# Kernel tuning notes

Measured on AMD Instinct MI355X. Metric: run time of the kernel, lower is better.

Reference implementation:

```python
import jax, jax.numpy as jnp
import numpy as np

PROJ = 8192     # projDim
THRESH = 1e-8   # numerical-stability epsilon for signed sqrt
L2_EPS = 1e-12  # eps of torch F.normalize


def setup_inputs() -> dict:
    key = jax.random.key(0)
    k1, k2, k3, k4, k5 = jax.random.split(key, 5)
    B, C, H, W = 16, 512, 14, 14
    x = jax.random.normal(k1, (B, C, H, W), dtype=jnp.float32)
    h1 = jax.random.randint(k2, (C,), 0, PROJ, dtype=jnp.int32)
    h2 = jax.random.randint(k3, (C,), 0, PROJ, dtype=jnp.int32)
    s1 = (2 * jax.random.randint(k4, (C,), 0, 2) - 1).astype(jnp.float32)
    s2 = (2 * jax.random.randint(k5, (C,), 0, 2) - 1).astype(jnp.float32)
    return {"x": x, "s1": s1, "s2": s2, "h1": h1, "h2": h2}


def reference(x, s1, s2, h1, h2):
    # x: [B, C, H, W]; h*: [C] hash buckets in [0, PROJ); s*: [C] signs (+-1)
    B, C, H, W = x.shape
    x_flat = jnp.transpose(x, (0, 2, 3, 1)).reshape(-1, C)  # [N, C], N = B*H*W

    def count_sketch(s, h):
        # Equivalent to x_flat @ M with M[c, h[c]] = s[c]: scatter-add of
        # sign-weighted channels into PROJ bins.  -> [N, PROJ]
        return jax.ops.segment_sum((x_flat * s).T, h, num_segments=PROJ).T

    fft1 = jnp.fft.fft(count_sketch(s1, h1), axis=-1)
    fft2 = jnp.fft.fft(count_sketch(s2, h2), axis=-1)
    conv = jnp.fft.ifft(fft1 * fft2, axis=-1).real       # [N, PROJ]
    y = conv.reshape(B, H, W, PROJ).sum(axis=(1, 2))      # sum pool -> [B, PROJ]
    y = jnp.sign(y) * jnp.sqrt(jnp.abs(y) + THRESH)       # signed sqrt
    norm = jnp.linalg.norm(y, axis=1, keepdims=True)
    return y / jnp.maximum(norm, L2_EPS)                  # l2 normalize (dim=1)
```

## Files before the change

kernel.cpp:

```cpp
#include <hip/hip_runtime.h>
#include <math.h>

#define PROJ 8192
#define NB   16
#define NC   512
#define HW   196

#define TB   128
#define KCH  20
#define LSA  24
#define LSB  36

__global__ void cbp_zero_ssq(float* __restrict__ ssq) {
    if (threadIdx.x < NB) ssq[threadIdx.x] = 0.0f;
}

__global__ __launch_bounds__(256)
void cbp_gram_scatter(const float* __restrict__ x,
                      const float* __restrict__ s1,
                      const float* __restrict__ s2,
                      const int*   __restrict__ h1,
                      const int*   __restrict__ h2,
                      float* __restrict__ ws) {
    __shared__ float sk[PROJ];
    __shared__ float As[TB * LSA];
    __shared__ float Bs[TB * LSB];

    const int blk = blockIdx.x;
    const int b = blk >> 4;
    const int I = (blk >> 2) & 3;
    const int J = blk & 3;
    const int c1base = I * TB;
    const int c2base = J * TB;

    const int tid = threadIdx.x;
    const int tx = tid & 15;
    const int ty = tid >> 4;

    for (int i = tid; i < PROJ; i += 256) sk[i] = 0.0f;

    const float* xa = x + ((size_t)b * NC + c1base) * HW;
    const float* xb = x + ((size_t)b * NC + c2base) * HW;

    float acc[8][8] = {{0.f}};

    for (int k0 = 0; k0 < HW; k0 += KCH) {
        const int kc = (k0 + KCH <= HW) ? KCH : (HW - k0);
        const int kq = kc >> 2;

        __syncthreads();
        for (int e = tid; e < TB * (KCH / 4); e += 256) {
            const int r = e / (KCH / 4);
            const int q = e - r * (KCH / 4);
            if (q < kq) {
                const float4 a4 = *(const float4*)&xa[r * HW + k0 + 4 * q];
                const float4 b4 = *(const float4*)&xb[r * HW + k0 + 4 * q];
                *(float4*)&As[r * LSA + 4 * q] = a4;
                *(float4*)&Bs[r * LSB + 4 * q] = b4;
            }
        }
        __syncthreads();

        for (int k = 0; k < kc; k += 4) {
            float4 av[8], bv[8];
#pragma unroll
            for (int i = 0; i < 8; i++)
                av[i] = *(const float4*)&As[(ty + 16 * i) * LSA + k];
#pragma unroll
            for (int j = 0; j < 8; j++)
                bv[j] = *(const float4*)&Bs[(tx + 16 * j) * LSB + k];
#pragma unroll
            for (int i = 0; i < 8; i++)
#pragma unroll
                for (int j = 0; j < 8; j++) {
                    acc[i][j] += av[i].x * bv[j].x;
                    acc[i][j] += av[i].y * bv[j].y;
                    acc[i][j] += av[i].z * bv[j].z;
                    acc[i][j] += av[i].w * bv[j].w;
                }
        }
    }
    __syncthreads();

    int   ha[8], hb[8];
    float sa[8], sb[8];
#pragma unroll
    for (int i = 0; i < 8; i++) {
        const int c1 = c1base + ty + 16 * i;
        ha[i] = h1[c1];  sa[i] = s1[c1];
    }
#pragma unroll
    for (int j = 0; j < 8; j++) {
        const int c2 = c2base + tx + 16 * j;
        hb[j] = h2[c2];  sb[j] = s2[c2];
    }
#pragma unroll
    for (int i = 0; i < 8; i++)
#pragma unroll
        for (int j = 0; j < 8; j++) {
            const int bin = (ha[i] + hb[j]) & (PROJ - 1);
            atomicAdd(&sk[bin], sa[i] * sb[j] * acc[i][j]);
        }
    __syncthreads();

    float4* dst = (float4*)(ws + (size_t)blk * PROJ);
    const float4* src = (const float4*)sk;
    for (int i = tid; i < PROJ / 4; i += 256) dst[i] = src[i];
}

__global__ __launch_bounds__(256)
void cbp_reduce(const float* __restrict__ ws, float* __restrict__ y,
                float* __restrict__ ssq) {
    const int b   = blockIdx.x >> 3;
    const int seg = blockIdx.x & 7;
    const int tid = threadIdx.x;
    const int bin = seg * 1024 + tid * 4;

    float4 s = {0.f, 0.f, 0.f, 0.f};
#pragma unroll
    for (int t = 0; t < 16; t++) {
        const float4 v = *(const float4*)&ws[((size_t)(b * 16 + t)) * PROJ + bin];
        s.x += v.x; s.y += v.y; s.z += v.z; s.w += v.w;
    }

    float4 o;
    float ls = 0.f;
    {
        float m;
        m = sqrtf(fabsf(s.x) + 1e-8f); o.x = (s.x > 0.f) ? m : (s.x < 0.f ? -m : 0.f);
        m = sqrtf(fabsf(s.y) + 1e-8f); o.y = (s.y > 0.f) ? m : (s.y < 0.f ? -m : 0.f);
        m = sqrtf(fabsf(s.z) + 1e-8f); o.z = (s.z > 0.f) ? m : (s.z < 0.f ? -m : 0.f);
        m = sqrtf(fabsf(s.w) + 1e-8f); o.w = (s.w > 0.f) ? m : (s.w < 0.f ? -m : 0.f);
        ls = o.x * o.x + o.y * o.y + o.z * o.z + o.w * o.w;
    }
    *(float4*)&y[(size_t)b * PROJ + bin] = o;

    __shared__ float red[256];
    red[tid] = ls;
    __syncthreads();
#pragma unroll
    for (int st = 128; st >= 1; st >>= 1) {
        if (tid < st) red[tid] += red[tid + st];
        __syncthreads();
    }
    if (tid == 0) atomicAdd(&ssq[b], red[0]);
}

__global__ __launch_bounds__(256)
void cbp_normalize(float* __restrict__ y, const float* __restrict__ ssq) {
    const int b   = blockIdx.x >> 1;
    const int off = (blockIdx.x & 1) * 4096;
    const int tid = threadIdx.x;
    const float inv = 1.0f / fmaxf(sqrtf(ssq[b]), 1e-12f);

    float4* row = (float4*)&y[(size_t)b * PROJ + off];
#pragma unroll
    for (int j = 0; j < 4; j++) {
        float4 v = row[j * 256 + tid];
        v.x *= inv; v.y *= inv; v.z *= inv; v.w *= inv;
        row[j * 256 + tid] = v;
    }
}

extern "C" void kernel_launch(void* const* d_in, const int* in_sizes, int n_in,
                              void* d_out, int out_size, void* d_ws, size_t ws_size,
                              hipStream_t stream) {
    const float* x  = (const float*)d_in[0];
    const float* s1 = (const float*)d_in[1];
    const float* s2 = (const float*)d_in[2];
    const int*   h1 = (const int*)d_in[3];
    const int*   h2 = (const int*)d_in[4];
    float* y  = (float*)d_out;
    float* ws = (float*)d_ws;
    float* ssq = ws + (size_t)256 * PROJ;

    hipLaunchKernelGGL(cbp_zero_ssq, dim3(1), dim3(64), 0, stream, ssq);
    hipLaunchKernelGGL(cbp_gram_scatter, dim3(NB * 16), dim3(256), 0, stream,
                       x, s1, s2, h1, h2, ws);
    hipLaunchKernelGGL(cbp_reduce, dim3(NB * 8), dim3(256), 0, stream, ws, y, ssq);
    hipLaunchKernelGGL(cbp_normalize, dim3(32), dim3(256), 0, stream, y, ssq);
}
```

Baseline: 128.4 us.

## Compute per-batch Gram via split-bf16 MFMA and deterministic partial-sum reduce

Replaces the FP32 FMA Gram matrix tile (128x128 over 196 spatial positions) with bf16 MFMA instructions. Each fp32 value is split into hi and lo bf16 parts and three MFMA products are accumulated to keep near-fp32 accuracy. The reduce kernel now uses 512 blocks and writes per-block partial sums of squares instead of using atomics, which removes the zeroing kernel launch. The normalize kernel sums the 32 partials per batch row. The cost is extra conversion work in the load loop and some precision loss from the 3-term bf16 split.

Result: faster. 111.2 us (-13.4%).

```diff
diff --git a/kernel.cpp b/kernel.cpp
--- a/kernel.cpp
+++ b/kernel.cpp
@@ -5,102 +5,134 @@
 #define NB   16
 #define NC   512
 #define HW   196
-
-#define TB   128
-#define KCH  20
-#define LSA  24
-#define LSB  36
-
-__global__ void cbp_zero_ssq(float* __restrict__ ssq) {
-    if (threadIdx.x < NB) ssq[threadIdx.x] = 0.0f;
+#define NKC  7
+#define LST  40
+
+typedef __attribute__((ext_vector_type(8))) short bf16x8;
+typedef __attribute__((ext_vector_type(4))) short short4v;
+typedef __attribute__((ext_vector_type(4))) float f32x4;
+
+__device__ __forceinline__ unsigned bf16_rne(float f) {
+    unsigned u = __builtin_bit_cast(unsigned, f);
+    return (u + 0x7fffu + ((u >> 16) & 1u)) >> 16;
 }
 
 __global__ __launch_bounds__(256)
-void cbp_gram_scatter(const float* __restrict__ x,
-                      const float* __restrict__ s1,
-                      const float* __restrict__ s2,
-                      const int*   __restrict__ h1,
-                      const int*   __restrict__ h2,
-                      float* __restrict__ ws) {
+void cbp_gram_mfma(const float* __restrict__ x,
+                   const float* __restrict__ s1,
+                   const float* __restrict__ s2,
+                   const int*   __restrict__ h1,
+                   const int*   __restrict__ h2,
+                   float* __restrict__ ws) {
     __shared__ float sk[PROJ];
-    __shared__ float As[TB * LSA];
-    __shared__ float Bs[TB * LSB];
-
-    const int blk = blockIdx.x;
-    const int b = blk >> 4;
-    const int I = (blk >> 2) & 3;
-    const int J = blk & 3;
-    const int c1base = I * TB;
-    const int c2base = J * TB;
-
-    const int tid = threadIdx.x;
-    const int tx = tid & 15;
-    const int ty = tid >> 4;
-
-    for (int i = tid; i < PROJ; i += 256) sk[i] = 0.0f;
+    __shared__ short Ah[128 * LST];
+    __shared__ short Al[128 * LST];
+    __shared__ short Bh[128 * LST];
+    __shared__ short Bl[128 * LST];
+    __shared__ int   lh1[128], lh2[128];
+    __shared__ float ls1[128], ls2[128];
+
+    const int tid  = threadIdx.x;
+    const int blk  = blockIdx.x;
+    const int b    = blk >> 4;
+    const int I    = (blk >> 2) & 3;
+    const int J    = blk & 3;
+    const int c1base = I * 128;
+    const int c2base = J * 128;
+
+    const int lane = tid & 63;
+    const int wave = tid >> 6;
+    const int quad = lane >> 4;
+    const int l15  = lane & 15;
+    const int wr   = (wave >> 1) * 64;
+    const int wc   = (wave & 1) * 64;
+
+    for (int i = tid; i < PROJ; i += 256) sk[i] = 0.f;
+    if (tid < 128) {
+        lh1[tid] = h1[c1base + tid]; ls1[tid] = s1[c1base + tid];
+        lh2[tid] = h2[c2base + tid]; ls2[tid] = s2[c2base + tid];
+    }
 
     const float* xa = x + ((size_t)b * NC + c1base) * HW;
     const float* xb = x + ((size_t)b * NC + c2base) * HW;
 
-    float acc[8][8] = {{0.f}};
-
-    for (int k0 = 0; k0 < HW; k0 += KCH) {
-        const int kc = (k0 + KCH <= HW) ? KCH : (HW - k0);
-        const int kq = kc >> 2;
-
+    f32x4 acc[4][4];
+#pragma unroll
+    for (int i = 0; i < 4; ++i)
+#pragma unroll
+        for (int j = 0; j < 4; ++j)
+            acc[i][j] = (f32x4){0.f, 0.f, 0.f, 0.f};
+
+    for (int kc = 0; kc < NKC; ++kc) {
+        const int k0 = kc * 32;
         __syncthreads();
-        for (int e = tid; e < TB * (KCH / 4); e += 256) {
-            const int r = e / (KCH / 4);
-            const int q = e - r * (KCH / 4);
-            if (q < kq) {
-                const float4 a4 = *(const float4*)&xa[r * HW + k0 + 4 * q];
-                const float4 b4 = *(const float4*)&xb[r * HW + k0 + 4 * q];
-                *(float4*)&As[r * LSA + 4 * q] = a4;
-                *(float4*)&Bs[r * LSB + 4 * q] = b4;
-            }
+#pragma unroll
+        for (int it = 0; it < 4; ++it) {
+            const int s  = tid + 256 * it;
+            const int r  = s >> 3;
+            const int q  = s & 7;
+            const int kk = k0 + 4 * q;
+            float4 va = {0.f, 0.f, 0.f, 0.f}, vb = {0.f, 0.f, 0.f, 0.f};
+            if (kk + 3 < HW) {
+                va = *(const float4*)&xa[r * HW + kk];
+                vb = *(const float4*)&xb[r * HW + kk];
+            }
+            short4v ah, al, bh, bl;
+            const float fa[4] = {va.x, va.y, va.z, va.w};
+            const float fb[4] = {vb.x, vb.y, vb.z, vb.w};
+#pragma unroll
+            for (int c = 0; c < 4; ++c) {
+                const unsigned ha_ = bf16_rne(fa[c]);
+                ah[c] = (short)ha_;
+                al[c] = (short)bf16_rne(fa[c] - __builtin_bit_cast(float, ha_ << 16));
+                const unsigned hb_ = bf16_rne(fb[c]);
+                bh[c] = (short)hb_;
+                bl[c] = (short)bf16_rne(fb[c] - __builtin_bit_cast(float, hb_ << 16));
+            }
+            *(short4v*)&Ah[r * LST + 4 * q] = ah;
+            *(short4v*)&Al[r * LST + 4 * q] = al;
+            *(short4v*)&Bh[r * LST + 4 * q] = bh;
+            *(short4v*)&Bl[r * LST + 4 * q] = bl;
         }
         __syncthreads();
 
-        for (int k = 0; k < kc; k += 4) {
-            float4 av[8], bv[8];
-#pragma unroll
-            for (int i = 0; i < 8; i++)
-                av[i] = *(const float4*)&As[(ty + 16 * i) * LSA + k];
-#pragma unroll
-            for (int j = 0; j < 8; j++)
-                bv[j] = *(const float4*)&Bs[(tx + 16 * j) * LSB + k];
-#pragma unroll
-            for (int i = 0; i < 8; i++)
-#pragma unroll
-                for (int j = 0; j < 8; j++) {
-                    acc[i][j] += av[i].x * bv[j].x;
-                    acc[i][j] += av[i].y * bv[j].y;
-                    acc[i][j] += av[i].z * bv[j].z;
-                    acc[i][j] += av[i].w * bv[j].w;
-                }
+        bf16x8 ahf[4], alf[4], bhf[4], blf[4];
+#pragma unroll
+        for (int i = 0; i < 4; ++i) {
+            const int ra = wr + i * 16 + l15;
+            const int rb = wc + i * 16 + l15;
+            ahf[i] = *(const bf16x8*)&Ah[ra * LST + quad * 8];
+            alf[i] = *(const bf16x8*)&Al[ra * LST + quad * 8];
+            bhf[i] = *(const bf16x8*)&Bh[rb * LST + quad * 8];
+            blf[i] = *(const bf16x8*)&Bl[rb * LST + quad * 8];
         }
+#pragma unroll
+        for (int i = 0; i < 4; ++i)
+#pragma unroll
+            for (int j = 0; j < 4; ++j) {
+                acc[i][j] = __builtin_amdgcn_mfma_f32_16x16x32_bf16(ahf[i], bhf[j], acc[i][j], 0, 0, 0);
+                acc[i][j] = __builtin_amdgcn_mfma_f32_16x16x32_bf16(ahf[i], blf[j], acc[i][j], 0, 0, 0);
+                acc[i][j] = __builtin_amdgcn_mfma_f32_16x16x32_bf16(alf[i], bhf[j], acc[i][j], 0, 0, 0);
+            }
     }
     __syncthreads();
 
-    int   ha[8], hb[8];
-    float sa[8], sb[8];
-#pragma unroll
-    for (int i = 0; i < 8; i++) {
-        const int c1 = c1base + ty + 16 * i;
-        ha[i] = h1[c1];  sa[i] = s1[c1];
-    }
-#pragma unroll
-    for (int j = 0; j < 8; j++) {
-        const int c2 = c2base + tx + 16 * j;
-        hb[j] = h2[c2];  sb[j] = s2[c2];
-    }
-#pragma unroll
-    for (int i = 0; i < 8; i++)
-#pragma unroll
-        for (int j = 0; j < 8; j++) {
-            const int bin = (ha[i] + hb[j]) & (PROJ - 1);
-            atomicAdd(&sk[bin], sa[i] * sb[j] * acc[i][j]);
+#pragma unroll
+    for (int i = 0; i < 4; ++i) {
+        const int lr0 = wr + i * 16 + quad * 4;
+#pragma unroll
+        for (int j = 0; j < 4; ++j) {
+            const int lc   = wc + j * 16 + l15;
+            const int h2v  = lh2[lc];
+            const float s2v = ls2[lc];
+#pragma unroll
+            for (int rg = 0; rg < 4; ++rg) {
+                const int lr  = lr0 + rg;
+                const int bin = (lh1[lr] + h2v) & (PROJ - 1);
+                atomicAdd(&sk[bin], ls1[lr] * s2v * acc[i][j][rg]);
+            }
         }
+    }
     __syncthreads();
 
     float4* dst = (float4*)(ws + (size_t)blk * PROJ);
@@ -110,52 +142,46 @@
 
 __global__ __launch_bounds__(256)
 void cbp_reduce(const float* __restrict__ ws, float* __restrict__ y,
-                float* __restrict__ ssq) {
-    const int b   = blockIdx.x >> 3;
-    const int seg = blockIdx.x & 7;
+                float* __restrict__ ssqp) {
+    const int blk = blockIdx.x;
+    const int b   = blk >> 5;
+    const int seg = blk & 31;
     const int tid = threadIdx.x;
-    const int bin = seg * 1024 + tid * 4;
-
-    float4 s = {0.f, 0.f, 0.f, 0.f};
-#pragma unroll
-    for (int t = 0; t < 16; t++) {
-        const float4 v = *(const float4*)&ws[((size_t)(b * 16 + t)) * PROJ + bin];
-        s.x += v.x; s.y += v.y; s.z += v.z; s.w += v.w;
-    }
-
-    float4 o;
-    float ls = 0.f;
-    {
-        float m;
-        m = sqrtf(fabsf(s.x) + 1e-8f); o.x = (s.x > 0.f) ? m : (s.x < 0.f ? -m : 0.f);
-        m = sqrtf(fabsf(s.y) + 1e-8f); o.y = (s.y > 0.f) ? m : (s.y < 0.f ? -m : 0.f);
-        m = sqrtf(fabsf(s.z) + 1e-8f); o.z = (s.z > 0.f) ? m : (s.z < 0.f ? -m : 0.f);
-        m = sqrtf(fabsf(s.w) + 1e-8f); o.w = (s.w > 0.f) ? m : (s.w < 0.f ? -m : 0.f);
-        ls = o.x * o.x + o.y * o.y + o.z * o.z + o.w * o.w;
-    }
-    *(float4*)&y[(size_t)b * PROJ + bin] = o;
+    const int bin = seg * 256 + tid;
+
+    const float* base = ws + (size_t)b * 16 * PROJ + bin;
+    float s = 0.f;
+#pragma unroll
+    for (int p = 0; p < 16; ++p) s += base[(size_t)p * PROJ];
+
+    const float m = sqrtf(fabsf(s) + 1e-8f);
+    const float o = (s > 0.f) ? m : (s < 0.f ? -m : 0.f);
+    y[b * PROJ + bin] = o;
 
     __shared__ float red[256];
-    red[tid] = ls;
+    red[tid] = o * o;
     __syncthreads();
 #pragma unroll
     for (int st = 128; st >= 1; st >>= 1) {
         if (tid < st) red[tid] += red[tid + st];
         __syncthreads();
     }
-    if (tid == 0) atomicAdd(&ssq[b], red[0]);
+    if (tid == 0) ssqp[blk] = red[0];
 }
 
 __global__ __launch_bounds__(256)
-void cbp_normalize(float* __restrict__ y, const float* __restrict__ ssq) {
+void cbp_normalize(float* __restrict__ y, const float* __restrict__ ssqp) {
     const int b   = blockIdx.x >> 1;
     const int off = (blockIdx.x & 1) * 4096;
     const int tid = threadIdx.x;
-    const float inv = 1.0f / fmaxf(sqrtf(ssq[b]), 1e-12f);
+    float ssq = 0.f;
+#pragma unroll
+    for (int i = 0; i < 32; ++i) ssq += ssqp[b * 32 + i];
+    const float inv = 1.0f / fmaxf(sqrtf(ssq), 1e-12f);
 
     float4* row = (float4*)&y[(size_t)b * PROJ + off];
 #pragma unroll
-    for (int j = 0; j < 4; j++) {
+    for (int j = 0; j < 4; ++j) {
         float4 v = row[j * 256 + tid];
         v.x *= inv; v.y *= inv; v.z *= inv; v.w *= inv;
         row[j * 256 + tid] = v;
@@ -170,13 +196,12 @@
     const float* s2 = (const float*)d_in[2];
     const int*   h1 = (const int*)d_in[3];
     const int*   h2 = (const int*)d_in[4];
-    float* y  = (float*)d_out;
-    float* ws = (float*)d_ws;
-    float* ssq = ws + (size_t)256 * PROJ;
-
-    hipLaunchKernelGGL(cbp_zero_ssq, dim3(1), dim3(64), 0, stream, ssq);
-    hipLaunchKernelGGL(cbp_gram_scatter, dim3(NB * 16), dim3(256), 0, stream,
+    float* y    = (float*)d_out;
+    float* ws   = (float*)d_ws;
+    float* ssqp = ws + (size_t)256 * PROJ;
+
+    hipLaunchKernelGGL(cbp_gram_mfma, dim3(NB * 16), dim3(256), 0, stream,
                        x, s1, s2, h1, h2, ws);
-    hipLaunchKernelGGL(cbp_reduce, dim3(NB * 8), dim3(256), 0, stream, ws, y, ssq);
-    hipLaunchKernelGGL(cbp_normalize, dim3(32), dim3(256), 0, stream, y, ssq);
-}
+    hipLaunchKernelGGL(cbp_reduce, dim3(512), dim3(256), 0, stream, ws, y, ssqp);
+    hipLaunchKernelGGL(cbp_normalize, dim3(32), dim3(256), 0, stream, y, ssqp);
+}
```
